# Performance work log

Hardware: AMD Instinct MI355X
Metric: run time of the kernel (lower is better)

Reference implementation:

```python
import jax, jax.numpy as jnp
import numpy as np

N = 100000   # atoms (nodes)
M = 1600000  # bonds (edges)
D = 64       # atom_fea_len


def setup_inputs() -> dict:
    key = jax.random.key(0)
    ks = jax.random.split(key, 8)
    atom_weights = jax.random.uniform(ks[0], (N, 1), dtype=jnp.float32)
    atom_in_fea = jax.random.normal(ks[1], (N, D), dtype=jnp.float32)
    self_fea_idx = jnp.sort(jax.random.randint(ks[2], (M,), 0, N))
    nbr_fea_idx = jax.random.randint(ks[3], (M,), 0, N)
    # message_nn: Linear(2D->D) + LeakyReLU + Linear(D->D)
    W1 = jax.random.normal(ks[4], (2 * D, D), dtype=jnp.float32) * (1.0 / np.sqrt(2 * D))
    b1 = jnp.zeros((D,), dtype=jnp.float32)
    W2 = jax.random.normal(ks[5], (D, D), dtype=jnp.float32) * (1.0 / np.sqrt(D))
    b2 = jnp.zeros((D,), dtype=jnp.float32)
    # pool_nn (gate): Linear(D->1)
    Wg = jax.random.normal(ks[6], (D, 1), dtype=jnp.float32) * (1.0 / np.sqrt(D))
    bg = jnp.zeros((1,), dtype=jnp.float32)
    return {"atom_weights": atom_weights, "atom_in_fea": atom_in_fea,
            "self_fea_idx": self_fea_idx, "nbr_fea_idx": nbr_fea_idx,
            "W1": W1, "b1": b1, "W2": W2, "b2": b2, "Wg": Wg, "bg": bg}


def reference(atom_weights, atom_in_fea, self_fea_idx, nbr_fea_idx,
              W1, b1, W2, b2, Wg, bg):
    n = atom_in_fea.shape[0]
    # gather-concat: [M, 2D]
    fea = jnp.concatenate([atom_in_fea[self_fea_idx], atom_in_fea[nbr_fea_idx]], axis=1)
    # message_nn MLP -> [M, D]
    fea = jax.nn.leaky_relu(fea @ W1 + b1) @ W2 + b2
    # weighted scatter-softmax attention pooling over segments self_fea_idx
    gate = fea @ Wg + bg                                    # [M, 1]
    gmax = jax.ops.segment_max(gate, self_fea_idx, num_segments=n)  # [N, 1]
    gate = jnp.exp(gate - gmax[self_fea_idx])
    gate = atom_weights[nbr_fea_idx] * gate                 # [M, 1]
    denom = jax.ops.segment_sum(gate, self_fea_idx, num_segments=n)  # [N, 1]
    gate = gate / (denom[self_fea_idx] + 1e-13)
    pooled = jax.ops.segment_sum(gate * fea, self_fea_idx, num_segments=n)  # [N, D]
    return pooled + atom_in_fea
```

## Files before the change

kernel.cpp:

```cpp
#include <hip/hip_runtime.h>
#include <math.h>

typedef float f32x4 __attribute__((ext_vector_type(4)));
typedef __bf16 bf16x8 __attribute__((ext_vector_type(8)));

__global__ void build_row_start(const int* __restrict__ self_idx,
                                int* __restrict__ row_start, int M, int N) {
  int i = blockIdx.x * blockDim.x + threadIdx.x;
  if (i >= M) return;
  int cur = self_idx[i];
  int prev = (i == 0) ? -1 : self_idx[i - 1];
  for (int j = prev + 1; j <= cur; ++j) row_start[j] = i;
  if (i == M - 1) {
    for (int j = cur + 1; j <= N; ++j) row_start[j] = M;
  }
}

__global__ __launch_bounds__(256, 2)
void precompute_uy(const float* __restrict__ atom_fea,
                   const float* __restrict__ W1,
                   const float* __restrict__ b1,
                   const float* __restrict__ W2,
                   __bf16* __restrict__ Ub, __bf16* __restrict__ Yb,
                   __bf16* __restrict__ W2pack, int N) {
  const int lane = threadIdx.x & 63;
  const int r16 = lane & 15, g = lane >> 4;
  const int wid = (blockIdx.x * blockDim.x + threadIdx.x) >> 6;
  const int nw = (gridDim.x * blockDim.x) >> 6;

  if (wid == 0) {
#pragma unroll
    for (int ks = 0; ks < 2; ++ks)
#pragma unroll
      for (int c = 0; c < 4; ++c) {
        bf16x8 t;
#pragma unroll
        for (int jj = 0; jj < 8; ++jj)
          t[jj] = (__bf16)W2[(size_t)(32 * ks + 8 * g + jj) * 64 + 16 * c + r16];
        *(bf16x8*)(W2pack + ((size_t)(ks * 4 + c) * 64 + lane) * 8) = t;
      }
  }

  bf16x8 wt[2][4], wb[2][4];
#pragma unroll
  for (int ks = 0; ks < 2; ++ks)
#pragma unroll
    for (int c = 0; c < 4; ++c) {
      bf16x8 t, b;
#pragma unroll
      for (int jj = 0; jj < 8; ++jj) {
        int k = 32 * ks + 8 * g + jj;
        t[jj] = (__bf16)W1[(size_t)k * 64 + 16 * c + r16];
        b[jj] = (__bf16)W1[(size_t)(64 + k) * 64 + 16 * c + r16];
      }
      wt[ks][c] = t; wb[ks][c] = b;
    }
  float b1c[4];
#pragma unroll
  for (int c = 0; c < 4; ++c) b1c[c] = b1[16 * c + r16];

  const int nTiles = (N + 15) >> 4;
  for (int tile = wid; tile < nTiles; tile += nw) {
    const int a0 = tile * 16;
    int arow = a0 + r16; if (arow >= N) arow = N - 1;

    bf16x8 af[2];
#pragma unroll
    for (int ks = 0; ks < 2; ++ks) {
      const float* p = atom_fea + (size_t)arow * 64 + 32 * ks + 8 * g;
      f32x4 x0 = *(const f32x4*)p;
      f32x4 x1 = *(const f32x4*)(p + 4);
      bf16x8 a;
#pragma unroll
      for (int jj = 0; jj < 4; ++jj) { a[jj] = (__bf16)x0[jj]; a[4 + jj] = (__bf16)x1[jj]; }
      af[ks] = a;
    }

    f32x4 uacc[4], yacc[4];
#pragma unroll
    for (int c = 0; c < 4; ++c) { uacc[c] = (f32x4)0.0f; yacc[c] = (f32x4)0.0f; }
#pragma unroll
    for (int ks = 0; ks < 2; ++ks)
#pragma unroll
      for (int c = 0; c < 4; ++c) {
        uacc[c] = __builtin_amdgcn_mfma_f32_16x16x32_bf16(af[ks], wt[ks][c], uacc[c], 0, 0, 0);
        yacc[c] = __builtin_amdgcn_mfma_f32_16x16x32_bf16(af[ks], wb[ks][c], yacc[c], 0, 0, 0);
      }

#pragma unroll
    for (int c = 0; c < 4; ++c)
#pragma unroll
      for (int j = 0; j < 4; ++j) {
        int row = a0 + 4 * g + j;
        if (row < N) {
          Ub[(size_t)row * 64 + 16 * c + r16] = (__bf16)(uacc[c][j] + b1c[c]);
          Yb[(size_t)row * 64 + 16 * c + r16] = (__bf16)yacc[c][j];
        }
      }
  }
}

__global__ __launch_bounds__(64, 3)
void fused_pool(const float* __restrict__ atom_w,
                const float* __restrict__ atom_fea,
                const int* __restrict__ nbr_idx,
                const float* __restrict__ W2,
                const float* __restrict__ b2,
                const float* __restrict__ Wg,
                const float* __restrict__ bg,
                const int* __restrict__ row_start,
                const __bf16* __restrict__ Ub,
                const __bf16* __restrict__ Yb,
                const __bf16* __restrict__ W2pack,
                float* __restrict__ out, int N) {
  const int lane = threadIdx.x & 63;
  const int r16 = lane & 15, g = lane >> 4;

  float wgl = 0.f;
  {
    const float* w2row = W2 + (size_t)lane * 64;
#pragma unroll
    for (int d = 0; d < 64; ++d) wgl = fmaf(w2row[d], Wg[d], wgl);
  }
  float wgsl[16];
#pragma unroll
  for (int ks = 0; ks < 2; ++ks)
#pragma unroll
    for (int jj = 0; jj < 8; ++jj)
      wgsl[ks * 8 + jj] = __shfl(wgl, 32 * ks + 8 * g + jj);

  float tb = b2[lane] * Wg[lane];
#pragma unroll
  for (int off = 1; off < 64; off <<= 1) tb += __shfl_xor(tb, off);
  const float bgp = bg[0] + tb;
  const float b2l = b2[lane];

  const int pstride = 2 * gridDim.x;
  for (int p0 = 2 * blockIdx.x; p0 < N; p0 += pstride) {
    const int sA = p0;
    const int sB = p0 + 1;
    const bool hasB = sB < N;

    const int startA = row_start[sA];
    const int endA = row_start[sA + 1];
    const int startB = hasB ? row_start[sB] : 0;
    const int endB = hasB ? row_start[sB + 1] : 0;

    float ufA[16], ufB[16];
    {
      const bf16x8 a0 = *(const bf16x8*)(Ub + (size_t)sA * 64 + 8 * g);
      const bf16x8 a1 = *(const bf16x8*)(Ub + (size_t)sA * 64 + 32 + 8 * g);
      const bf16x8 c0 = hasB ? *(const bf16x8*)(Ub + (size_t)sB * 64 + 8 * g) : a0;
      const bf16x8 c1 = hasB ? *(const bf16x8*)(Ub + (size_t)sB * 64 + 32 + 8 * g) : a1;
#pragma unroll
      for (int jj = 0; jj < 8; ++jj) {
        ufA[jj] = (float)a0[jj]; ufA[8 + jj] = (float)a1[jj];
        ufB[jj] = (float)c0[jj]; ufB[8 + jj] = (float)c1[jj];
      }
    }

    float zA[16], zB[16];
#pragma unroll
    for (int k = 0; k < 16; ++k) { zA[k] = 0.f; zB[k] = 0.f; }
    float wsumA = 0.f, wsumB = 0.f;

    const int nTA = (endA - startA + 15) >> 4;
    const int nTB = (endB - startB + 15) >> 4;
    const int nT = nTA > nTB ? nTA : nTB;

    for (int t = 0; t < nT; ++t) {
      const int baseA = startA + 16 * t;
      const int baseB = startB + 16 * t;
      const bool actA = baseA < endA;
      const bool actB = hasB && baseB < endB;

      int nbA = 0; bf16x8 yA0 = {}, yA1 = {}; float awA = 0.f; bool vA = false;
      int nbB = 0; bf16x8 yB0 = {}, yB1 = {}; float awB = 0.f; bool vB = false;
      if (actA) {
        const int e = baseA + r16; vA = e < endA;
        nbA = vA ? nbr_idx[e] : 0;
        const __bf16* yr = Yb + ((size_t)nbA << 6);
        yA0 = *(const bf16x8*)(yr + 8 * g);
        yA1 = *(const bf16x8*)(yr + 32 + 8 * g);
        awA = atom_w[nbA];
      }
      if (actB) {
        const int e = baseB + r16; vB = e < endB;
        nbB = vB ? nbr_idx[e] : 0;
        const __bf16* yr = Yb + ((size_t)nbB << 6);
        yB0 = *(const bf16x8*)(yr + 8 * g);
        yB1 = *(const bf16x8*)(yr + 32 + 8 * g);
        awB = atom_w[nbB];
      }

      if (actA) {
        float hf[16];
#pragma unroll
        for (int jj = 0; jj < 8; ++jj) {
          float a = ufA[jj] + (float)yA0[jj];
          float b = ufA[8 + jj] + (float)yA1[jj];
          hf[jj] = fmaxf(a, 0.01f * a);
          hf[8 + jj] = fmaxf(b, 0.01f * b);
        }
        float pacc = 0.f;
#pragma unroll
        for (int i = 0; i < 16; ++i) pacc = fmaf(hf[i], wgsl[i], pacc);
        pacc += __shfl_xor(pacc, 16);
        pacc += __shfl_xor(pacc, 32);
        const float w = vA ? awA * __expf(pacc + bgp) : 0.f;
        wsumA += w;
#pragma unroll
        for (int k = 0; k < 16; ++k) zA[k] = fmaf(w, hf[k], zA[k]);
      }
      if (actB) {
        float hf[16];
#pragma unroll
        for (int jj = 0; jj < 8; ++jj) {
          float a = ufB[jj] + (float)yB0[jj];
          float b = ufB[8 + jj] + (float)yB1[jj];
          hf[jj] = fmaxf(a, 0.01f * a);
          hf[8 + jj] = fmaxf(b, 0.01f * b);
        }
        float pacc = 0.f;
#pragma unroll
        for (int i = 0; i < 16; ++i) pacc = fmaf(hf[i], wgsl[i], pacc);
        pacc += __shfl_xor(pacc, 16);
        pacc += __shfl_xor(pacc, 32);
        const float w = vB ? awB * __expf(pacc + bgp) : 0.f;
        wsumB += w;
#pragma unroll
        for (int k = 0; k < 16; ++k) zB[k] = fmaf(w, hf[k], zB[k]);
      }
    }

    const float xrA = atom_fea[(size_t)sA * 64 + lane];
    const float xrB = hasB ? atom_fea[(size_t)sB * 64 + lane] : 0.f;

    bf16x8 zfA0, zfA1, zfB0, zfB1;
#pragma unroll
    for (int jj = 0; jj < 8; ++jj) {
      zfA0[jj] = (__bf16)zA[jj]; zfA1[jj] = (__bf16)zA[8 + jj];
      zfB0[jj] = (__bf16)zB[jj]; zfB1[jj] = (__bf16)zB[8 + jj];
    }

    f32x4 fA[4], fB[4];
#pragma unroll
    for (int c = 0; c < 4; ++c) { fA[c] = (f32x4)0.0f; fB[c] = (f32x4)0.0f; }
#pragma unroll
    for (int c = 0; c < 4; ++c) {
      const bf16x8 wf0 = *(const bf16x8*)(W2pack + ((size_t)(0 * 4 + c) * 64 + lane) * 8);
      const bf16x8 wf1 = *(const bf16x8*)(W2pack + ((size_t)(1 * 4 + c) * 64 + lane) * 8);
      fA[c] = __builtin_amdgcn_mfma_f32_16x16x32_bf16(zfA0, wf0, fA[c], 0, 0, 0);
      fA[c] = __builtin_amdgcn_mfma_f32_16x16x32_bf16(zfA1, wf1, fA[c], 0, 0, 0);
      fB[c] = __builtin_amdgcn_mfma_f32_16x16x32_bf16(zfB0, wf0, fB[c], 0, 0, 0);
      fB[c] = __builtin_amdgcn_mfma_f32_16x16x32_bf16(zfB1, wf1, fB[c], 0, 0, 0);
    }

    float avA[4], avB[4];
#pragma unroll
    for (int c = 0; c < 4; ++c) {
      float a = (fA[c][0] + fA[c][1]) + (fA[c][2] + fA[c][3]);
      float b = (fB[c][0] + fB[c][1]) + (fB[c][2] + fB[c][3]);
      a += __shfl_xor(a, 16); b += __shfl_xor(b, 16);
      a += __shfl_xor(a, 32); b += __shfl_xor(b, 32);
      avA[c] = a; avB[c] = b;
    }
    float ssA = wsumA, ssB = wsumB;
#pragma unroll
    for (int off = 1; off < 16; off <<= 1) {
      ssA += __shfl_xor(ssA, off);
      ssB += __shfl_xor(ssB, off);
    }

    float valA = avA[0];
    valA = (g == 1) ? avA[1] : valA;
    valA = (g == 2) ? avA[2] : valA;
    valA = (g == 3) ? avA[3] : valA;
    valA = fmaf(ssA, b2l, valA);
    out[(size_t)sA * 64 + lane] = valA / (ssA + 1e-13f) + xrA;

    if (hasB) {
      float valB = avB[0];
      valB = (g == 1) ? avB[1] : valB;
      valB = (g == 2) ? avB[2] : valB;
      valB = (g == 3) ? avB[3] : valB;
      valB = fmaf(ssB, b2l, valB);
      out[(size_t)sB * 64 + lane] = valB / (ssB + 1e-13f) + xrB;
    }
  }
}

extern "C" void kernel_launch(void* const* d_in, const int* in_sizes, int n_in,
                              void* d_out, int out_size, void* d_ws, size_t ws_size,
                              hipStream_t stream) {
  const float* atom_w   = (const float*)d_in[0];
  const float* atom_fea = (const float*)d_in[1];
  const int*   self_idx = (const int*)d_in[2];
  const int*   nbr_idx  = (const int*)d_in[3];
  const float* W1 = (const float*)d_in[4];
  const float* b1 = (const float*)d_in[5];
  const float* W2 = (const float*)d_in[6];
  const float* b2 = (const float*)d_in[7];
  const float* Wg = (const float*)d_in[8];
  const float* bg = (const float*)d_in[9];
  float* out = (float*)d_out;

  const int N = in_sizes[0];
  const int M = in_sizes[2];

  char* ws = (char*)d_ws;
  int* row_start = (int*)ws;
  size_t off = ((size_t)(N + 1) * sizeof(int) + 255) & ~(size_t)255;
  __bf16* W2pack = (__bf16*)(ws + off);
  __bf16* Ub = W2pack + 8 * 64 * 8;
  __bf16* Yb = Ub + (size_t)N * 64;

  hipLaunchKernelGGL(build_row_start, dim3((M + 255) / 256), dim3(256), 0,
                     stream, self_idx, row_start, M, N);
  hipLaunchKernelGGL(precompute_uy, dim3(512), dim3(256), 0, stream,
                     atom_fea, W1, b1, W2, Ub, Yb, W2pack, N);
  hipLaunchKernelGGL(fused_pool, dim3(8192), dim3(64), 0, stream,
                     atom_w, atom_fea, nbr_idx, W2, b2, Wg, bg,
                     row_start, Ub, Yb, W2pack, out, N);
}
```

Measured before the change: 122.2 us.

## Prefetch next segment pair's row bounds, U rows and residuals in fused_pool

```diff
diff --git a/kernel.cpp b/kernel.cpp
--- a/kernel.cpp
+++ b/kernel.cpp
@@ -100,7 +100,7 @@
   }
 }
 
-__global__ __launch_bounds__(64, 3)
+__global__ __launch_bounds__(64, 4)
 void fused_pool(const float* __restrict__ atom_w,
                 const float* __restrict__ atom_fea,
                 const int* __restrict__ nbr_idx,
@@ -136,33 +136,47 @@
   const float b2l = b2[lane];
 
   const int pstride = 2 * gridDim.x;
-  for (int p0 = 2 * blockIdx.x; p0 < N; p0 += pstride) {
-    const int sA = p0;
-    const int sB = p0 + 1;
+  int p = 2 * blockIdx.x;
+
+  int nrs0 = 0, nrs1 = 0, nrs2 = 0;
+  bf16x8 nuA0 = {}, nuA1 = {}, nuB0 = {}, nuB1 = {};
+  float nxrA = 0.f, nxrB = 0.f;
+
+  auto issue_head = [&](int pp) {
+    if (pp < N) {
+      nrs0 = row_start[pp];
+      nrs1 = row_start[pp + 1];
+      const int i2 = (pp + 2 <= N) ? (pp + 2) : N;
+      nrs2 = row_start[i2];
+      const int pb = (pp + 1 < N) ? (pp + 1) : pp;
+      nuA0 = *(const bf16x8*)(Ub + (size_t)pp * 64 + 8 * g);
+      nuA1 = *(const bf16x8*)(Ub + (size_t)pp * 64 + 32 + 8 * g);
+      nuB0 = *(const bf16x8*)(Ub + (size_t)pb * 64 + 8 * g);
+      nuB1 = *(const bf16x8*)(Ub + (size_t)pb * 64 + 32 + 8 * g);
+      nxrA = atom_fea[(size_t)pp * 64 + lane];
+      nxrB = atom_fea[(size_t)pb * 64 + lane];
+    }
+  };
+
+  issue_head(p);
+
+  for (; p < N; p += pstride) {
+    const int sA = p, sB = p + 1;
     const bool hasB = sB < N;
 
-    const int startA = row_start[sA];
-    const int endA = row_start[sA + 1];
-    const int startB = hasB ? row_start[sB] : 0;
-    const int endB = hasB ? row_start[sB + 1] : 0;
-
-    float ufA[16], ufB[16];
-    {
-      const bf16x8 a0 = *(const bf16x8*)(Ub + (size_t)sA * 64 + 8 * g);
-      const bf16x8 a1 = *(const bf16x8*)(Ub + (size_t)sA * 64 + 32 + 8 * g);
-      const bf16x8 c0 = hasB ? *(const bf16x8*)(Ub + (size_t)sB * 64 + 8 * g) : a0;
-      const bf16x8 c1 = hasB ? *(const bf16x8*)(Ub + (size_t)sB * 64 + 32 + 8 * g) : a1;
-#pragma unroll
-      for (int jj = 0; jj < 8; ++jj) {
-        ufA[jj] = (float)a0[jj]; ufA[8 + jj] = (float)a1[jj];
-        ufB[jj] = (float)c0[jj]; ufB[8 + jj] = (float)c1[jj];
-      }
-    }
+    const int startA = nrs0;
+    const int endA = nrs1;
+    const int startB = endA;
+    const int endB = hasB ? nrs2 : endA;
+    const bf16x8 uA0 = nuA0, uA1 = nuA1, uB0 = nuB0, uB1 = nuB1;
+    const float xrA = nxrA, xrB = nxrB;
+
+    issue_head(p + pstride);
 
     float zA[16], zB[16];
 #pragma unroll
     for (int k = 0; k < 16; ++k) { zA[k] = 0.f; zB[k] = 0.f; }
-    float wsumA = 0.f, wsumB = 0.f;
+    float wsA = 0.f, wsB = 0.f;
 
     const int nTA = (endA - startA + 15) >> 4;
     const int nTB = (endB - startB + 15) >> 4;
@@ -172,10 +186,11 @@
       const int baseA = startA + 16 * t;
       const int baseB = startB + 16 * t;
       const bool actA = baseA < endA;
-      const bool actB = hasB && baseB < endB;
-
-      int nbA = 0; bf16x8 yA0 = {}, yA1 = {}; float awA = 0.f; bool vA = false;
-      int nbB = 0; bf16x8 yB0 = {}, yB1 = {}; float awB = 0.f; bool vB = false;
+      const bool actB = baseB < endB;
+
+      int nbA = 0, nbB = 0; bool vA = false, vB = false;
+      bf16x8 yA0 = {}, yA1 = {}, yB0 = {}, yB1 = {};
+      float awA = 0.f, awB = 0.f;
       if (actA) {
         const int e = baseA + r16; vA = e < endA;
         nbA = vA ? nbr_idx[e] : 0;
@@ -193,48 +208,49 @@
         awB = atom_w[nbB];
       }
 
+      float hfA[16], hfB[16];
+      float pA = 0.f, pB = 0.f;
       if (actA) {
-        float hf[16];
 #pragma unroll
         for (int jj = 0; jj < 8; ++jj) {
-          float a = ufA[jj] + (float)yA0[jj];
-          float b = ufA[8 + jj] + (float)yA1[jj];
-          hf[jj] = fmaxf(a, 0.01f * a);
-          hf[8 + jj] = fmaxf(b, 0.01f * b);
+          float a = (float)uA0[jj] + (float)yA0[jj];
+          float b = (float)uA1[jj] + (float)yA1[jj];
+          hfA[jj] = fmaxf(a, 0.01f * a);
+          hfA[8 + jj] = fmaxf(b, 0.01f * b);
         }
-        float pacc = 0.f;
-#pragma unroll
-        for (int i = 0; i < 16; ++i) pacc = fmaf(hf[i], wgsl[i], pacc);
-        pacc += __shfl_xor(pacc, 16);
-        pacc += __shfl_xor(pacc, 32);
-        const float w = vA ? awA * __expf(pacc + bgp) : 0.f;
-        wsumA += w;
-#pragma unroll
-        for (int k = 0; k < 16; ++k) zA[k] = fmaf(w, hf[k], zA[k]);
+#pragma unroll
+        for (int i = 0; i < 16; ++i) pA = fmaf(hfA[i], wgsl[i], pA);
       }
       if (actB) {
-        float hf[16];
 #pragma unroll
         for (int jj = 0; jj < 8; ++jj) {
-          float a = ufB[jj] + (float)yB0[jj];
-          float b = ufB[8 + jj] + (float)yB1[jj];
-          hf[jj] = fmaxf(a, 0.01f * a);
-          hf[8 + jj] = fmaxf(b, 0.01f * b);
+          float a = (float)uB0[jj] + (float)yB0[jj];
+          float b = (float)uB1[jj] + (float)yB1[jj];
+          hfB[jj] = fmaxf(a, 0.01f * a);
+          hfB[8 + jj] = fmaxf(b, 0.01f * b);
         }
-        float pacc = 0.f;
-#pragma unroll
-        for (int i = 0; i < 16; ++i) pacc = fmaf(hf[i], wgsl[i], pacc);
-        pacc += __shfl_xor(pacc, 16);
-        pacc += __shfl_xor(pacc, 32);
-        const float w = vB ? awB * __expf(pacc + bgp) : 0.f;
-        wsumB += w;
-#pragma unroll
-        for (int k = 0; k < 16; ++k) zB[k] = fmaf(w, hf[k], zB[k]);
-      }
-    }
-
-    const float xrA = atom_fea[(size_t)sA * 64 + lane];
-    const float xrB = hasB ? atom_fea[(size_t)sB * 64 + lane] : 0.f;
+#pragma unroll
+        for (int i = 0; i < 16; ++i) pB = fmaf(hfB[i], wgsl[i], pB);
+      }
+
+      pA += __shfl_xor(pA, 16);
+      pB += __shfl_xor(pB, 16);
+      pA += __shfl_xor(pA, 32);
+      pB += __shfl_xor(pB, 32);
+
+      if (actA) {
+        const float w = vA ? awA * __expf(pA + bgp) : 0.f;
+        wsA += w;
+#pragma unroll
+        for (int k = 0; k < 16; ++k) zA[k] = fmaf(w, hfA[k], zA[k]);
+      }
+      if (actB) {
+        const float w = vB ? awB * __expf(pB + bgp) : 0.f;
+        wsB += w;
+#pragma unroll
+        for (int k = 0; k < 16; ++k) zB[k] = fmaf(w, hfB[k], zB[k]);
+      }
+    }
 
     bf16x8 zfA0, zfA1, zfB0, zfB1;
 #pragma unroll
@@ -265,7 +281,7 @@
       a += __shfl_xor(a, 32); b += __shfl_xor(b, 32);
       avA[c] = a; avB[c] = b;
     }
-    float ssA = wsumA, ssB = wsumB;
+    float ssA = wsA, ssB = wsB;
 #pragma unroll
     for (int off = 1; off < 16; off <<= 1) {
       ssA += __shfl_xor(ssA, off);
```

New measurement: 369.1 us. 3.02x slower.
